# Kernel tuning notes

Measured on AMD Instinct MI355X. Metric: run time of the kernel, lower is better.

Reference implementation:

```python
import jax, jax.numpy as jnp
import numpy as np


def _apply_rope(t, cos, sin):
    # t: [b, s, h, d]; cos/sin: [s, d//2]; interleaved complex rotation
    b, s, h, d = t.shape
    tr = t.reshape(b, s, h, d // 2, 2)
    a, bb = tr[..., 0], tr[..., 1]
    c = cos[None, :, None, :]
    si = sin[None, :, None, :]
    out_r = a * c - bb * si
    out_i = a * si + bb * c
    return jnp.stack([out_r, out_i], axis=-1).reshape(b, s, h, d)


def setup_inputs() -> dict:
    key = jax.random.key(0)
    ks = jax.random.split(key, 10)
    B, S, D = 4, 512, 4096
    H, HKV, HD = 32, 8, 128
    START = 512
    wscale = 0.02  # keep activations in sane range
    x = jax.random.normal(ks[0], (B, S, D), dtype=jnp.float32)
    wq = jax.random.normal(ks[1], (H * HD, D), dtype=jnp.float32) * wscale
    wk = jax.random.normal(ks[2], (HKV * HD, D), dtype=jnp.float32) * wscale
    wv = jax.random.normal(ks[3], (HKV * HD, D), dtype=jnp.float32) * wscale
    wo = jax.random.normal(ks[4], (D, H * HD), dtype=jnp.float32) * wscale
    # RoPE angles for absolute positions [START, START+S)
    theta = 500000.0
    inv_freq = 1.0 / (theta ** (np.arange(0, HD, 2, dtype=np.float32) / HD))
    pos = np.arange(START, START + S, dtype=np.float32)
    ang = pos[:, None] * inv_freq[None, :]  # [S, HD//2]
    freqs_cos = jnp.asarray(np.cos(ang), dtype=jnp.float32)
    freqs_sin = jnp.asarray(np.sin(ang), dtype=jnp.float32)
    cache_k = jax.random.normal(ks[5], (B, START, HKV, HD), dtype=jnp.float32)
    cache_v = jax.random.normal(ks[6], (B, START, HKV, HD), dtype=jnp.float32)
    return {"x": x, "wq": wq, "wk": wk, "wv": wv, "wo": wo,
            "freqs_cos": freqs_cos, "freqs_sin": freqs_sin,
            "cache_k": cache_k, "cache_v": cache_v, "start_pos": START}


def reference(x, wq, wk, wv, wo, freqs_cos, freqs_sin, cache_k, cache_v, start_pos):
    B, S, D = x.shape
    H = wq.shape[0] // 128
    HKV = wk.shape[0] // 128
    HD = 128
    n_rep = H // HKV
    # QKV projections (Linear: y = x @ W^T)
    xq = jnp.einsum('bsd,ed->bse', x, wq).reshape(B, S, H, HD)
    xk = jnp.einsum('bsd,ed->bse', x, wk).reshape(B, S, HKV, HD)
    xv = jnp.einsum('bsd,ed->bse', x, wv).reshape(B, S, HKV, HD)
    # rotary embedding on new q/k
    xq = _apply_rope(xq, freqs_cos, freqs_sin)
    xk = _apply_rope(xk, freqs_cos, freqs_sin)
    # append new k/v to cache -> total kv length T = start_pos + S
    keys = jnp.concatenate([cache_k, xk], axis=1)    # [B, T, HKV, HD]
    values = jnp.concatenate([cache_v, xv], axis=1)  # [B, T, HKV, HD]
    # GQA: repeat kv heads (repeat_interleave along head dim)
    keys = jnp.repeat(keys, n_rep, axis=2)      # [B, T, H, HD]
    values = jnp.repeat(values, n_rep, axis=2)  # [B, T, H, HD]
    scores = jnp.einsum('bqhd,bkhd->bhqk', xq, keys) / jnp.sqrt(jnp.float32(HD))
    # causal mask: query abs pos start_pos+i attends to kv pos <= start_pos+i
    T = start_pos + S
    q_pos = start_pos + jnp.arange(S)
    k_pos = jnp.arange(T)
    mask = k_pos[None, :] <= q_pos[:, None]  # [S, T]
    scores = jnp.where(mask[None, None, :, :], scores, -jnp.inf)
    probs = jax.nn.softmax(scores.astype(jnp.float32), axis=-1).astype(x.dtype)
    out = jnp.einsum('bhqk,bkhd->bqhd', probs, values).reshape(B, S, H * HD)
    return jnp.einsum('bse,de->bsd', out, wo)
```

## Files before the change

### kernel.cpp

```cpp
#include <hip/hip_runtime.h>
#include <hip/hip_bf16.h>


#define B_ 4
#define S_ 512
#define D_ 4096
#define H_ 32
#define HKV_ 8
#define HD_ 128
#define T_ 1024
#define M_ 2048
#define NQKV_ 6144

typedef __attribute__((ext_vector_type(8))) short bf16x8;
typedef __attribute__((ext_vector_type(4))) float f32x4;

#define GLOAD_LDS16(g, l)                                                     \
  __builtin_amdgcn_global_load_lds(                                           \
      (const __attribute__((address_space(1))) void*)(g),                     \
      (__attribute__((address_space(3))) void*)(l), 16, 0, 0)

__global__ void cvt_f32_bf16(const float* __restrict__ in,
                             __hip_bfloat16* __restrict__ out, long n) {
  long i = ((long)blockIdx.x * blockDim.x + threadIdx.x) * 4;
  if (i >= n) return;
  float4 v = *(const float4*)(in + i);
  __hip_bfloat16 t[4] = {__float2bfloat16(v.x), __float2bfloat16(v.y),
                         __float2bfloat16(v.z), __float2bfloat16(v.w)};
  *(uint2*)(out + i) = *(const uint2*)t;
}

__global__ __launch_bounds__(512, 2) void gemm_qkv(
    const __hip_bfloat16* __restrict__ A, const __hip_bfloat16* __restrict__ B,
    float* __restrict__ C, int K, long ldA, long ldB, long ldC) {
  const int lin = blockIdx.x + 32 * blockIdx.y;
  const int swz = (lin & 7) * 32 + (lin >> 3);
  const int m0 = (swz >> 5) << 8;
  const int n0 = (swz & 31) * 192;

  const int tid = threadIdx.x;
  const int w = tid >> 6, l = tid & 63;
  const int wm = w >> 2, wn = w & 3;
  const int lr = l & 15, lq = l >> 4;

  __shared__ __align__(16) __hip_bfloat16 smem[2][28672];

  const int rS = w * 8 + (l >> 3);
  const int cS = (l & 7) ^ (l >> 3);
  const __hip_bfloat16* gA = A + (long)(m0 + rS) * ldA + cS * 8;
  const __hip_bfloat16* gB = B + (long)(n0 + rS) * ldB + cS * 8;
  const int wofs = w * 512;

  const int sl0 = (lq ^ (lr & 7)) * 8;
  const int sl1 = ((4 + lq) ^ (lr & 7)) * 8;
  const int aRow = (wm * 128 + lr) * 64;
  const int bRow = (wn * 48 + lr) * 64;

  f32x4 acc[8][3];
#pragma unroll
  for (int i = 0; i < 8; i++)
#pragma unroll
    for (int j = 0; j < 3; j++) acc[i][j] = f32x4{0.f, 0.f, 0.f, 0.f};

  const int nkt = K >> 6;

#define STAGEQ(buf, ko)                                              \
  {                                                                  \
    GLOAD_LDS16(gA + (ko), &smem[buf][wofs]);                        \
    GLOAD_LDS16(gA + 64 * ldA + (ko), &smem[buf][4096 + wofs]);      \
    GLOAD_LDS16(gA + 128 * ldA + (ko), &smem[buf][8192 + wofs]);     \
    GLOAD_LDS16(gA + 192 * ldA + (ko), &smem[buf][12288 + wofs]);    \
    GLOAD_LDS16(gB + (ko), &smem[buf][16384 + wofs]);                \
    GLOAD_LDS16(gB + 64 * ldB + (ko), &smem[buf][20480 + wofs]);     \
    GLOAD_LDS16(gB + 128 * ldB + (ko), &smem[buf][24576 + wofs]);    \
  }

  STAGEQ(0, 0);
  asm volatile("s_waitcnt vmcnt(0)" ::: "memory");
  __builtin_amdgcn_s_barrier();

  bf16x8 af[4], bfr[3];
  for (int t = 0; t < nkt; ++t) {
    const int bc = t & 1;
    int tn = t + 1;
    if (tn == nkt) tn = 0;
    const long ko = (long)tn << 6;
    const __hip_bfloat16* rA = &smem[bc][0];
    const __hip_bfloat16* rB = &smem[bc][16384];

#pragma unroll
    for (int i = 0; i < 4; i++)
      af[i] = *(const bf16x8*)(rA + aRow + i * 1024 + sl0);
#pragma unroll
    for (int j = 0; j < 3; j++)
      bfr[j] = *(const bf16x8*)(rB + bRow + j * 1024 + sl0);
    STAGEQ(bc ^ 1, ko);
    __builtin_amdgcn_s_barrier();
    __builtin_amdgcn_s_setprio(1);
#pragma unroll
    for (int i = 0; i < 4; i++)
#pragma unroll
      for (int j = 0; j < 3; j++)
        acc[i][j] = __builtin_amdgcn_mfma_f32_16x16x32_bf16(af[i], bfr[j],
                                                            acc[i][j], 0, 0, 0);
    __builtin_amdgcn_s_setprio(0);
    __builtin_amdgcn_s_barrier();

#pragma unroll
    for (int i = 0; i < 4; i++)
      af[i] = *(const bf16x8*)(rA + aRow + (i + 4) * 1024 + sl0);
    __builtin_amdgcn_s_barrier();
    __builtin_amdgcn_s_setprio(1);
#pragma unroll
    for (int i = 0; i < 4; i++)
#pragma unroll
      for (int j = 0; j < 3; j++)
        acc[i + 4][j] = __builtin_amdgcn_mfma_f32_16x16x32_bf16(
            af[i], bfr[j], acc[i + 4][j], 0, 0, 0);
    __builtin_amdgcn_s_setprio(0);
    __builtin_amdgcn_s_barrier();

#pragma unroll
    for (int i = 0; i < 4; i++)
      af[i] = *(const bf16x8*)(rA + aRow + i * 1024 + sl1);
#pragma unroll
    for (int j = 0; j < 3; j++)
      bfr[j] = *(const bf16x8*)(rB + bRow + j * 1024 + sl1);
    __builtin_amdgcn_s_barrier();
    __builtin_amdgcn_s_setprio(1);
#pragma unroll
    for (int i = 0; i < 4; i++)
#pragma unroll
      for (int j = 0; j < 3; j++)
        acc[i][j] = __builtin_amdgcn_mfma_f32_16x16x32_bf16(af[i], bfr[j],
                                                            acc[i][j], 0, 0, 0);
    __builtin_amdgcn_s_setprio(0);
    __builtin_amdgcn_s_barrier();

#pragma unroll
    for (int i = 0; i < 4; i++)
      af[i] = *(const bf16x8*)(rA + aRow + (i + 4) * 1024 + sl1);
    __builtin_amdgcn_s_barrier();
    __builtin_amdgcn_s_setprio(1);
#pragma unroll
    for (int i = 0; i < 4; i++)
#pragma unroll
      for (int j = 0; j < 3; j++)
        acc[i + 4][j] = __builtin_amdgcn_mfma_f32_16x16x32_bf16(
            af[i], bfr[j], acc[i + 4][j], 0, 0, 0);
    __builtin_amdgcn_s_setprio(0);
    asm volatile("s_waitcnt vmcnt(0)" ::: "memory");
    __builtin_amdgcn_s_barrier();
  }

#undef STAGEQ

  const int crow = m0 + wm * 128 + lq * 4;
  const int ccol = n0 + wn * 48 + lr;
#pragma unroll
  for (int i = 0; i < 8; i++)
#pragma unroll
    for (int j = 0; j < 3; j++)
#pragma unroll
      for (int r = 0; r < 4; r++)
        C[(long)(crow + i * 16 + r) * ldC + (ccol + j * 16)] = acc[i][j][r];
}

__global__ __launch_bounds__(512, 2) void gemm128(
    const __hip_bfloat16* __restrict__ A, const __hip_bfloat16* __restrict__ B,
    float* __restrict__ C, int M, int N, int K, long ldA, long ldB, long ldC) {
  const int nbx = N >> 8;
  const int nwg = nbx * (M >> 7);
  const int lin = blockIdx.x + nbx * blockIdx.y;
  const int cpx = nwg >> 3;
  const int swz = (lin & 7) * cpx + (lin >> 3);
  const int by = swz / nbx;
  const int m0 = by << 7;
  const int n0 = (swz - by * nbx) << 8;

  const int tid = threadIdx.x;
  const int w = tid >> 6, l = tid & 63;
  const int wm = w >> 2, wn = w & 3;
  const int lr = l & 15, lq = l >> 4;

  __shared__ __align__(16) __hip_bfloat16 smem[3][24576];

  const int rS = w * 16 + (l >> 2);
  const int cS = (l & 3) ^ ((rS >> 1) & 3);
  const __hip_bfloat16* gA = A + (long)(m0 + rS) * ldA + cS * 8;
  const __hip_bfloat16* gB = B + (long)(n0 + rS) * ldB + cS * 8;
  const long stB = 128 * ldB;
  const int wofs = w * 512;

  const int cR = (lq ^ ((lr >> 1) & 3)) * 8;
  const int aOff = (wm * 64 + lr) * 32 + cR;
  const int bOff = (wn * 64 + lr) * 32 + cR;

  f32x4 acc[4][4];
#pragma unroll
  for (int i = 0; i < 4; i++)
#pragma unroll
    for (int j = 0; j < 4; j++) acc[i][j] = f32x4{0.f, 0.f, 0.f, 0.f};

  const int nkt = K >> 6;

#define STAGEF(buf, ko)                                            \
  {                                                                \
    const __hip_bfloat16* ga_ = gA + (ko);                         \
    GLOAD_LDS16(ga_, &smem[buf][wofs]);                            \
    GLOAD_LDS16(ga_ + 32, &smem[buf][4096 + wofs]);                \
    const __hip_bfloat16* gb_ = gB + (ko);                         \
    GLOAD_LDS16(gb_, &smem[buf][8192 + wofs]);                     \
    GLOAD_LDS16(gb_ + stB, &smem[buf][12288 + wofs]);              \
    GLOAD_LDS16(gb_ + 32, &smem[buf][16384 + wofs]);               \
    GLOAD_LDS16(gb_ + stB + 32, &smem[buf][20480 + wofs]);         \
  }

  STAGEF(0, 0);
  STAGEF(1, 64);
  asm volatile("s_waitcnt vmcnt(6)" ::: "memory");
  __builtin_amdgcn_s_barrier();

  int bc = 0, b1 = 1, b2 = 2;
  bf16x8 af[4], bfr[4];
  for (int t = 0; t < nkt; ++t) {
    int t2 = t + 2;
    if (t2 >= nkt) t2 -= nkt;
    const long ko2 = (long)t2 << 6;
    STAGEF(b2, ko2);

    const __hip_bfloat16* rA = &smem[bc][0];
    const __hip_bfloat16* rB = &smem[bc][8192];

#pragma unroll
    for (int i = 0; i < 4; i++) af[i] = *(const bf16x8*)(rA + aOff + i * 512);
#pragma unroll
    for (int j = 0; j < 4; j++) bfr[j] = *(const bf16x8*)(rB + bOff + j * 512);
    __builtin_amdgcn_s_setprio(1);
#pragma unroll
    for (int i = 0; i < 4; i++)
#pragma unroll
      for (int j = 0; j < 4; j++)
        acc[i][j] = __builtin_amdgcn_mfma_f32_16x16x32_bf16(af[i], bfr[j],
                                                            acc[i][j], 0, 0, 0);
    __builtin_amdgcn_s_setprio(0);

#pragma unroll
    for (int i = 0; i < 4; i++)
      af[i] = *(const bf16x8*)(rA + 4096 + aOff + i * 512);
#pragma unroll
    for (int j = 0; j < 4; j++)
      bfr[j] = *(const bf16x8*)(rB + 8192 + bOff + j * 512);
    __builtin_amdgcn_s_setprio(1);
#pragma unroll
    for (int i = 0; i < 4; i++)
#pragma unroll
      for (int j = 0; j < 4; j++)
        acc[i][j] = __builtin_amdgcn_mfma_f32_16x16x32_bf16(af[i], bfr[j],
                                                            acc[i][j], 0, 0, 0);
    __builtin_amdgcn_s_setprio(0);

    asm volatile("s_waitcnt lgkmcnt(0)" ::: "memory");
    __builtin_amdgcn_sched_barrier(0);
    asm volatile("s_waitcnt vmcnt(6)" ::: "memory");
    __builtin_amdgcn_s_barrier();

    int tmp = bc; bc = b1; b1 = b2; b2 = tmp;
  }
  asm volatile("s_waitcnt vmcnt(0)" ::: "memory");

#undef STAGEF

  const int crow = m0 + wm * 64 + lq * 4;
  const int ccol = n0 + wn * 64 + lr;
#pragma unroll
  for (int i = 0; i < 4; i++)
#pragma unroll
    for (int j = 0; j < 4; j++)
#pragma unroll
      for (int r = 0; r < 4; r++)
        C[(long)(crow + i * 16 + r) * ldC + (ccol + j * 16)] = acc[i][j][r];
}

__global__ __launch_bounds__(256, 2) void flash_attn(
    const __hip_bfloat16* __restrict__ qb,
    const __hip_bfloat16* __restrict__ kb,
    const __hip_bfloat16* __restrict__ vtb,
    __hip_bfloat16* __restrict__ ob) {
  const int qt = 3 - blockIdx.x;
  const int z = blockIdx.y;
  const int b = z >> 5, h = z & 31, kvh = h >> 2;
  const int q0 = qt * 128;
  const int tid = threadIdx.x, wave = tid >> 6, lane = tid & 63;
  const int lr = lane & 15, lq = lane >> 4;
  const int wrow = wave * 32;
  const float scale = 0.08838834764831845f;

  __shared__ __align__(16) __hip_bfloat16 smem[64 * 128 + 128 * 64 + 128 * 72];
  __hip_bfloat16* Ks = smem;
  __hip_bfloat16* Vs = smem + 64 * 128;
  __hip_bfloat16* Ps = smem + 64 * 128 + 128 * 64;
  __hip_bfloat16* Os = smem;

  const __hip_bfloat16* Kz = kb + ((long)(b * 8 + kvh)) * T_ * HD_;
  const __hip_bfloat16* Vz = vtb + ((long)(b * 8 + kvh)) * HD_ * T_;
  const __hip_bfloat16* Qz = qb + ((long)(b * 512 + q0)) * 4096 + h * 128;
  __hip_bfloat16* obz = ob + ((long)(b * 512 + q0)) * 4096 + h * 128;

  bf16x8 qf[2][4];
#pragma unroll
  for (int i = 0; i < 2; i++)
#pragma unroll
    for (int kb4 = 0; kb4 < 4; kb4++)
      qf[i][kb4] = *(const bf16x8*)(Qz + (long)(wrow + i * 16 + lr) * 4096 +
                                    kb4 * 32 + lq * 8);

  int kOff[4], vOff[4];
#pragma unroll
  for (int it = 0; it < 4; it++) {
    int G = it * 256 + tid;
    int t = G >> 4, ck = (G & 15) ^ (t & 7);
    kOff[it] = t * 128 + ck * 8;
    int d = G >> 3, cv = (G & 7) ^ (d & 7);
    vOff[it] = d * 1024 + cv * 8;
  }

  f32x4 O[2][8];
#pragma unroll
  for (int i = 0; i < 2; i++)
#pragma unroll
    for (int j = 0; j < 8; j++) O[i][j] = f32x4{0.f, 0.f, 0.f, 0.f};
  float mst[2][4], lst[2][4];
#pragma unroll
  for (int i = 0; i < 2; i++)
#pragma unroll
    for (int r = 0; r < 4; r++) {
      mst[i][r] = -1e30f;
      lst[i][r] = 0.f;
    }

  const int ntiles = 10 + 2 * qt, fulltiles = 8 + 2 * qt;
  const int hxor = lr & 7;

  bf16x8 kreg[4], vreg[4];
#pragma unroll
  for (int it = 0; it < 4; it++)
    kreg[it] = *(const bf16x8*)(Kz + kOff[it]);
#pragma unroll
  for (int it = 0; it < 4; it++)
    vreg[it] = *(const bf16x8*)(Vz + vOff[it]);

  for (int kt = 0; kt < ntiles; kt++) {
    const int k0 = kt * 64;
#pragma unroll
    for (int it = 0; it < 4; it++)
      *(bf16x8*)(Ks + (it * 256 + tid) * 8) = kreg[it];
#pragma unroll
    for (int it = 0; it < 4; it++)
      *(bf16x8*)(Vs + (it * 256 + tid) * 8) = vreg[it];
    if (kt + 1 < ntiles) {
      const long kn = (long)(kt + 1) * 64;
#pragma unroll
      for (int it = 0; it < 4; it++)
        kreg[it] = *(const bf16x8*)(Kz + kn * 128 + kOff[it]);
#pragma unroll
      for (int it = 0; it < 4; it++)
        vreg[it] = *(const bf16x8*)(Vz + kn + vOff[it]);
    }
    asm volatile("s_waitcnt lgkmcnt(0)" ::: "memory");
    __builtin_amdgcn_s_barrier();

    f32x4 s[2][4];
#pragma unroll
    for (int i = 0; i < 2; i++)
#pragma unroll
      for (int j = 0; j < 4; j++) s[i][j] = f32x4{0.f, 0.f, 0.f, 0.f};
#pragma unroll
    for (int kb4 = 0; kb4 < 4; kb4++) {
      bf16x8 kf[4];
#pragma unroll
      for (int j = 0; j < 4; j++)
        kf[j] = *(const bf16x8*)(Ks + (j * 16 + lr) * 128 +
                                 ((kb4 * 4 + lq) ^ hxor) * 8);
#pragma unroll
      for (int i = 0; i < 2; i++)
#pragma unroll
        for (int j = 0; j < 4; j++)
          s[i][j] = __builtin_amdgcn_mfma_f32_16x16x32_bf16(qf[i][kb4], kf[j],
                                                            s[i][j], 0, 0, 0);
    }

    const bool mt = (kt >= fulltiles);
#pragma unroll
    for (int i = 0; i < 2; i++)
#pragma unroll
      for (int j = 0; j < 4; j++)
#pragma unroll
        for (int r = 0; r < 4; r++) {
          float sv = s[i][j][r] * scale;
          if (mt) {
            int key = k0 + j * 16 + lr;
            int qp = 512 + q0 + wrow + i * 16 + lq * 4 + r;
            if (key > qp) sv = -1e30f;
          }
          s[i][j][r] = sv;
        }

    float al[2][4];
#pragma unroll
    for (int i = 0; i < 2; i++)
#pragma unroll
      for (int r = 0; r < 4; r++) {
        float mx = fmaxf(fmaxf(s[i][0][r], s[i][1][r]),
                         fmaxf(s[i][2][r], s[i][3][r]));
        mx = fmaxf(mx, __shfl_xor(mx, 1));
        mx = fmaxf(mx, __shfl_xor(mx, 2));
        mx = fmaxf(mx, __shfl_xor(mx, 4));
        mx = fmaxf(mx, __shfl_xor(mx, 8));
        float mn = fmaxf(mst[i][r], mx);
        al[i][r] = __expf(mst[i][r] - mn);
        mst[i][r] = mn;
      }
#pragma unroll
    for (int i = 0; i < 2; i++)
#pragma unroll
      for (int j = 0; j < 4; j++)
#pragma unroll
        for (int r = 0; r < 4; r++)
          s[i][j][r] = __expf(s[i][j][r] - mst[i][r]);
#pragma unroll
    for (int i = 0; i < 2; i++)
#pragma unroll
      for (int r = 0; r < 4; r++) {
        float sm = s[i][0][r] + s[i][1][r] + s[i][2][r] + s[i][3][r];
        sm += __shfl_xor(sm, 1);
        sm += __shfl_xor(sm, 2);
        sm += __shfl_xor(sm, 4);
        sm += __shfl_xor(sm, 8);
        lst[i][r] = lst[i][r] * al[i][r] + sm;
      }
#pragma unroll
    for (int i = 0; i < 2; i++)
#pragma unroll
      for (int j = 0; j < 8; j++)
#pragma unroll
        for (int r = 0; r < 4; r++) O[i][j][r] *= al[i][r];

#pragma unroll
    for (int i = 0; i < 2; i++)
#pragma unroll
      for (int j = 0; j < 4; j++)
#pragma unroll
        for (int r = 0; r < 4; r++)
          Ps[(wrow + i * 16 + lq * 4 + r) * 72 + j * 16 + lr] =
              __float2bfloat16(s[i][j][r]);

#pragma unroll
    for (int kc = 0; kc < 2; kc++) {
      bf16x8 pa[2];
#pragma unroll
      for (int i = 0; i < 2; i++)
        pa[i] = *(const bf16x8*)(Ps + (wrow + i * 16 + lr) * 72 + kc * 32 +
                                 lq * 8);
      bf16x8 vf[8];
#pragma unroll
      for (int j = 0; j < 8; j++)
        vf[j] = *(const bf16x8*)(Vs + (j * 16 + lr) * 64 +
                                 ((kc * 4 + lq) ^ hxor) * 8);
#pragma unroll
      for (int i = 0; i < 2; i++)
#pragma unroll
        for (int j = 0; j < 8; j++)
          O[i][j] = __builtin_amdgcn_mfma_f32_16x16x32_bf16(pa[i], vf[j],
                                                            O[i][j], 0, 0, 0);
    }
    asm volatile("s_waitcnt lgkmcnt(0)" ::: "memory");
    __builtin_amdgcn_s_barrier();
  }

#pragma unroll
  for (int i = 0; i < 2; i++)
#pragma unroll
    for (int r = 0; r < 4; r++) {
      float inv = 1.f / lst[i][r];
#pragma unroll
      for (int j = 0; j < 8; j++)
        Os[(wrow + i * 16 + lq * 4 + r) * 136 + j * 16 + lr] =
            __float2bfloat16(O[i][j][r] * inv);
    }
  __syncthreads();
#pragma unroll
  for (int it = 0; it < 8; it++) {
    int G = it * 256 + tid;
    int m = G >> 4, c = G & 15;
    *(bf16x8*)(obz + (long)m * 4096 + c * 8) =
        *(const bf16x8*)(Os + m * 136 + c * 8);
  }
}

__global__ void rope_kernel(const float* __restrict__ qkv,
                            const float* __restrict__ fcos,
                            const float* __restrict__ fsin,
                            __hip_bfloat16* __restrict__ qb,
                            __hip_bfloat16* __restrict__ kb) {
  int m = blockIdx.y;
  int j = blockIdx.x * blockDim.x + threadIdx.x;
  if (j >= 2560) return;
  int s = m & (S_ - 1);
  long rowbase = (long)m * NQKV_;
  if (j < 2048) {
    int dpair = j & 63;
    float a = qkv[rowbase + 2 * j], bb = qkv[rowbase + 2 * j + 1];
    float c = fcos[s * 64 + dpair], si = fsin[s * 64 + dpair];
    long o = (long)m * 4096 + 2 * j;
    qb[o] = __float2bfloat16(a * c - bb * si);
    qb[o + 1] = __float2bfloat16(a * si + bb * c);
  } else {
    int j2 = j - 2048;
    int kvh = j2 >> 6, dpair = j2 & 63;
    float a = qkv[rowbase + 4096 + 2 * j2], bb = qkv[rowbase + 4096 + 2 * j2 + 1];
    float c = fcos[s * 64 + dpair], si = fsin[s * 64 + dpair];
    int b = m >> 9;
    long o = (((long)(b * HKV_ + kvh)) * T_ + 512 + s) * HD_ + 2 * dpair;
    kb[o] = __float2bfloat16(a * c - bb * si);
    kb[o + 1] = __float2bfloat16(a * si + bb * c);
  }
}

__global__ void kcache_cvt(const float* __restrict__ cache_k,
                           __hip_bfloat16* __restrict__ kb) {
  long i = (long)blockIdx.x * 256 + threadIdx.x;
  if (i >= (long)B_ * HKV_ * 512 * HD_) return;
  int d = i & 127;
  int t = (i >> 7) & 511;
  int kvh = (i >> 16) & 7;
  int b = i >> 19;
  long o = (((long)(b * HKV_ + kvh)) * T_ + t) * HD_ + d;
  kb[o] = __float2bfloat16(
      cache_k[(((long)(b * 512 + t)) * HKV_ + kvh) * HD_ + d]);
}

__global__ void v_transpose(const float* __restrict__ cache_v,
                            const float* __restrict__ qkv,
                            __hip_bfloat16* __restrict__ vtb) {
  __shared__ float tile[32][33];
  int t0 = blockIdx.x * 32, d0 = blockIdx.y * 32;
  int bk = blockIdx.z;
  int b = bk >> 3, kvh = bk & 7;
#pragma unroll
  for (int it = 0; it < 4; it++) {
    int t = t0 + threadIdx.y + it * 8;
    int d = d0 + threadIdx.x;
    float v;
    if (t < 512)
      v = cache_v[(((long)(b * 512 + t)) * HKV_ + kvh) * HD_ + d];
    else
      v = qkv[((long)(b * S_) + (t - 512)) * NQKV_ + 5120 + kvh * HD_ + d];
    tile[threadIdx.y + it * 8][threadIdx.x] = v;
  }
  __syncthreads();
#pragma unroll
  for (int it = 0; it < 4; it++) {
    int d = d0 + threadIdx.y + it * 8;
    int t = t0 + threadIdx.x;
    vtb[((long)bk * HD_ + d) * T_ + t] =
        __float2bfloat16(tile[threadIdx.x][threadIdx.y + it * 8]);
  }
}

extern "C" void kernel_launch(void* const* d_in, const int* in_sizes, int n_in,
                              void* d_out, int out_size, void* d_ws,
                              size_t ws_size, hipStream_t stream) {
  const float* x = (const float*)d_in[0];
  const float* wq = (const float*)d_in[1];
  const float* wk = (const float*)d_in[2];
  const float* wv = (const float*)d_in[3];
  const float* wo = (const float*)d_in[4];
  const float* fcos = (const float*)d_in[5];
  const float* fsin = (const float*)d_in[6];
  const float* cache_k = (const float*)d_in[7];
  const float* cache_v = (const float*)d_in[8];
  float* out = (float*)d_out;

  char* ws = (char*)d_ws;
  const size_t szR0 = (size_t)M_ * 4096 * 2;
  const size_t szR1 = (size_t)NQKV_ * D_ * 2;
  const size_t szR2 = (size_t)M_ * NQKV_ * 4;
  const size_t szKV = (size_t)B_ * HKV_ * T_ * HD_ * 2;

  size_t R0 = 0;
  size_t R1 = R0 + szR0;
  size_t R2 = R1 + szR1;
  size_t R3 = R2 + szR2;
  size_t R4 = R3 + szKV;

  __hip_bfloat16* xb = (__hip_bfloat16*)(ws + R0);
  __hip_bfloat16* wqkvb = (__hip_bfloat16*)(ws + R1);
  float* qkvf = (float*)(ws + R2);
  __hip_bfloat16* kb = (__hip_bfloat16*)(ws + R3);
  __hip_bfloat16* vtb = (__hip_bfloat16*)(ws + R4);

  dim3 blk(256);

  cvt_f32_bf16<<<(M_ * (long)D_ / 4 + 255) / 256, blk, 0, stream>>>(
      x, xb, (long)M_ * D_);
  cvt_f32_bf16<<<((long)D_ * D_ / 4 + 255) / 256, blk, 0, stream>>>(
      wq, wqkvb, (long)D_ * D_);
  cvt_f32_bf16<<<((long)1024 * D_ / 4 + 255) / 256, blk, 0, stream>>>(
      wk, wqkvb + (long)4096 * D_, (long)1024 * D_);
  cvt_f32_bf16<<<((long)1024 * D_ / 4 + 255) / 256, blk, 0, stream>>>(
      wv, wqkvb + (long)5120 * D_, (long)1024 * D_);

  gemm_qkv<<<dim3(32, 8), dim3(512), 0, stream>>>(
      xb, wqkvb, qkvf, D_, D_, D_, NQKV_);

  __hip_bfloat16* qb = xb;
  rope_kernel<<<dim3(10, M_), blk, 0, stream>>>(qkvf, fcos, fsin, qb, kb);

  kcache_cvt<<<((long)B_ * HKV_ * 512 * HD_ + 255) / 256, blk, 0, stream>>>(
      cache_k, kb);
  v_transpose<<<dim3(T_ / 32, HD_ / 32, B_ * HKV_), dim3(32, 8), 0, stream>>>(
      cache_v, qkvf, vtb);

  __hip_bfloat16* wob = wqkvb;
  cvt_f32_bf16<<<((long)D_ * D_ / 4 + 255) / 256, blk, 0, stream>>>(
      wo, wob, (long)D_ * D_);

  __hip_bfloat16* ob = xb;
  flash_attn<<<dim3(4, B_ * H_), blk, 0, stream>>>(qb, kb, vtb, ob);

  gemm128<<<dim3(D_ / 256, M_ / 128), dim3(512), 0, stream>>>(
      ob, wob, out, M_, D_, D_, D_, D_, D_);
}
```

Measured before the change: 500.0 us.

## Shrink attention query tile to 64, load K/V direct-to-LDS, lazy softmax rescale, fuse weight converts

Flash attention now uses 64-query tiles (one 16-row MFMA block per wave) with twice as many blocks and a 4-blocks-per-CU launch bound. The P buffer reuses the K region to cut shared memory. K/V tiles load with global_load_lds instead of register prefetch, which drops the software pipelining and adds an extra barrier per tile. Softmax skips the running-max rescale while the new max stays within 8 of the old one. The three Q/K/V weight conversions become a single kernel launch.

```diff
diff --git a/kernel.cpp b/kernel.cpp
--- a/kernel.cpp
+++ b/kernel.cpp
@@ -25,6 +25,27 @@
   long i = ((long)blockIdx.x * blockDim.x + threadIdx.x) * 4;
   if (i >= n) return;
   float4 v = *(const float4*)(in + i);
+  __hip_bfloat16 t[4] = {__float2bfloat16(v.x), __float2bfloat16(v.y),
+                         __float2bfloat16(v.z), __float2bfloat16(v.w)};
+  *(uint2*)(out + i) = *(const uint2*)t;
+}
+
+__global__ void cvt_wqkv(const float* __restrict__ wq,
+                         const float* __restrict__ wk,
+                         const float* __restrict__ wv,
+                         __hip_bfloat16* __restrict__ out) {
+  long i = ((long)blockIdx.x * 256 + threadIdx.x) * 4;
+  long row = i >> 12;
+  const float* src;
+  long off;
+  if (row < 4096) {
+    src = wq; off = i;
+  } else if (row < 5120) {
+    src = wk; off = i - (long)4096 * 4096;
+  } else {
+    src = wv; off = i - (long)5120 * 4096;
+  }
+  float4 v = *(const float4*)(src + off);
   __hip_bfloat16 t[4] = {__float2bfloat16(v.x), __float2bfloat16(v.y),
                          __float2bfloat16(v.z), __float2bfloat16(v.w)};
   *(uint2*)(out + i) = *(const uint2*)t;
@@ -282,24 +303,24 @@
         C[(long)(crow + i * 16 + r) * ldC + (ccol + j * 16)] = acc[i][j][r];
 }
 
-__global__ __launch_bounds__(256, 2) void flash_attn(
+__global__ __launch_bounds__(256, 4) void flash_attn(
     const __hip_bfloat16* __restrict__ qb,
     const __hip_bfloat16* __restrict__ kb,
     const __hip_bfloat16* __restrict__ vtb,
     __hip_bfloat16* __restrict__ ob) {
-  const int qt = 3 - blockIdx.x;
+  const int qt = 7 - blockIdx.x;
   const int z = blockIdx.y;
   const int b = z >> 5, h = z & 31, kvh = h >> 2;
-  const int q0 = qt * 128;
+  const int q0 = qt * 64;
   const int tid = threadIdx.x, wave = tid >> 6, lane = tid & 63;
   const int lr = lane & 15, lq = lane >> 4;
-  const int wrow = wave * 32;
+  const int wrow = wave * 16;
   const float scale = 0.08838834764831845f;
 
-  __shared__ __align__(16) __hip_bfloat16 smem[64 * 128 + 128 * 64 + 128 * 72];
+  __shared__ __align__(16) __hip_bfloat16 smem[64 * 128 + 128 * 64];
   __hip_bfloat16* Ks = smem;
   __hip_bfloat16* Vs = smem + 64 * 128;
-  __hip_bfloat16* Ps = smem + 64 * 128 + 128 * 64;
+  __hip_bfloat16* Ps = smem;
   __hip_bfloat16* Os = smem;
 
   const __hip_bfloat16* Kz = kb + ((long)(b * 8 + kvh)) * T_ * HD_;
@@ -307,13 +328,11 @@
   const __hip_bfloat16* Qz = qb + ((long)(b * 512 + q0)) * 4096 + h * 128;
   __hip_bfloat16* obz = ob + ((long)(b * 512 + q0)) * 4096 + h * 128;
 
-  bf16x8 qf[2][4];
-#pragma unroll
-  for (int i = 0; i < 2; i++)
-#pragma unroll
-    for (int kb4 = 0; kb4 < 4; kb4++)
-      qf[i][kb4] = *(const bf16x8*)(Qz + (long)(wrow + i * 16 + lr) * 4096 +
-                                    kb4 * 32 + lq * 8);
+  bf16x8 qf[4];
+#pragma unroll
+  for (int kb4 = 0; kb4 < 4; kb4++)
+    qf[kb4] = *(const bf16x8*)(Qz + (long)(wrow + lr) * 4096 + kb4 * 32 +
+                               lq * 8);
 
   int kOff[4], vOff[4];
 #pragma unroll
@@ -325,56 +344,33 @@
     vOff[it] = d * 1024 + cv * 8;
   }
 
-  f32x4 O[2][8];
-#pragma unroll
-  for (int i = 0; i < 2; i++)
-#pragma unroll
-    for (int j = 0; j < 8; j++) O[i][j] = f32x4{0.f, 0.f, 0.f, 0.f};
-  float mst[2][4], lst[2][4];
-#pragma unroll
-  for (int i = 0; i < 2; i++)
-#pragma unroll
-    for (int r = 0; r < 4; r++) {
-      mst[i][r] = -1e30f;
-      lst[i][r] = 0.f;
-    }
-
-  const int ntiles = 10 + 2 * qt, fulltiles = 8 + 2 * qt;
+  f32x4 O[8];
+#pragma unroll
+  for (int j = 0; j < 8; j++) O[j] = f32x4{0.f, 0.f, 0.f, 0.f};
+  float mst[4], lst[4];
+#pragma unroll
+  for (int r = 0; r < 4; r++) {
+    mst[r] = -1e30f;
+    lst[r] = 0.f;
+  }
+
+  const int ntiles = 9 + qt, fulltiles = 8 + qt;
   const int hxor = lr & 7;
-
-  bf16x8 kreg[4], vreg[4];
-#pragma unroll
-  for (int it = 0; it < 4; it++)
-    kreg[it] = *(const bf16x8*)(Kz + kOff[it]);
-#pragma unroll
-  for (int it = 0; it < 4; it++)
-    vreg[it] = *(const bf16x8*)(Vz + vOff[it]);
 
   for (int kt = 0; kt < ntiles; kt++) {
     const int k0 = kt * 64;
 #pragma unroll
     for (int it = 0; it < 4; it++)
-      *(bf16x8*)(Ks + (it * 256 + tid) * 8) = kreg[it];
+      GLOAD_LDS16(Kz + (long)k0 * 128 + kOff[it],
+                  Ks + (it * 256 + wave * 64) * 8);
 #pragma unroll
     for (int it = 0; it < 4; it++)
-      *(bf16x8*)(Vs + (it * 256 + tid) * 8) = vreg[it];
-    if (kt + 1 < ntiles) {
-      const long kn = (long)(kt + 1) * 64;
-#pragma unroll
-      for (int it = 0; it < 4; it++)
-        kreg[it] = *(const bf16x8*)(Kz + kn * 128 + kOff[it]);
-#pragma unroll
-      for (int it = 0; it < 4; it++)
-        vreg[it] = *(const bf16x8*)(Vz + kn + vOff[it]);
-    }
-    asm volatile("s_waitcnt lgkmcnt(0)" ::: "memory");
-    __builtin_amdgcn_s_barrier();
-
-    f32x4 s[2][4];
-#pragma unroll
-    for (int i = 0; i < 2; i++)
-#pragma unroll
-      for (int j = 0; j < 4; j++) s[i][j] = f32x4{0.f, 0.f, 0.f, 0.f};
+      GLOAD_LDS16(Vz + k0 + vOff[it], Vs + (it * 256 + wave * 64) * 8);
+    __syncthreads();
+
+    f32x4 s[4];
+#pragma unroll
+    for (int j = 0; j < 4; j++) s[j] = f32x4{0.f, 0.f, 0.f, 0.f};
 #pragma unroll
     for (int kb4 = 0; kb4 < 4; kb4++) {
       bf16x8 kf[4];
@@ -383,114 +379,113 @@
         kf[j] = *(const bf16x8*)(Ks + (j * 16 + lr) * 128 +
                                  ((kb4 * 4 + lq) ^ hxor) * 8);
 #pragma unroll
-      for (int i = 0; i < 2; i++)
-#pragma unroll
-        for (int j = 0; j < 4; j++)
-          s[i][j] = __builtin_amdgcn_mfma_f32_16x16x32_bf16(qf[i][kb4], kf[j],
-                                                            s[i][j], 0, 0, 0);
+      for (int j = 0; j < 4; j++)
+        s[j] = __builtin_amdgcn_mfma_f32_16x16x32_bf16(qf[kb4], kf[j], s[j],
+                                                       0, 0, 0);
     }
+    __syncthreads();
 
     const bool mt = (kt >= fulltiles);
 #pragma unroll
-    for (int i = 0; i < 2; i++)
+    for (int j = 0; j < 4; j++)
+#pragma unroll
+      for (int r = 0; r < 4; r++) {
+        float sv = s[j][r] * scale;
+        if (mt) {
+          int key = k0 + j * 16 + lr;
+          int qp = 512 + q0 + wrow + lq * 4 + r;
+          if (key > qp) sv = -1e30f;
+        }
+        s[j][r] = sv;
+      }
+
+    float mx[4];
+    bool ok = true;
+#pragma unroll
+    for (int r = 0; r < 4; r++) {
+      float m = fmaxf(fmaxf(s[0][r], s[1][r]), fmaxf(s[2][r], s[3][r]));
+      m = fmaxf(m, __shfl_xor(m, 1));
+      m = fmaxf(m, __shfl_xor(m, 2));
+      m = fmaxf(m, __shfl_xor(m, 4));
+      m = fmaxf(m, __shfl_xor(m, 8));
+      mx[r] = m;
+      ok = ok && (m - mst[r] <= 8.f);
+    }
+    if (__all(ok)) {
 #pragma unroll
       for (int j = 0; j < 4; j++)
 #pragma unroll
-        for (int r = 0; r < 4; r++) {
-          float sv = s[i][j][r] * scale;
-          if (mt) {
-            int key = k0 + j * 16 + lr;
-            int qp = 512 + q0 + wrow + i * 16 + lq * 4 + r;
-            if (key > qp) sv = -1e30f;
-          }
-          s[i][j][r] = sv;
-        }
-
-    float al[2][4];
-#pragma unroll
-    for (int i = 0; i < 2; i++)
+        for (int r = 0; r < 4; r++) s[j][r] = __expf(s[j][r] - mst[r]);
 #pragma unroll
       for (int r = 0; r < 4; r++) {
-        float mx = fmaxf(fmaxf(s[i][0][r], s[i][1][r]),
-                         fmaxf(s[i][2][r], s[i][3][r]));
-        mx = fmaxf(mx, __shfl_xor(mx, 1));
-        mx = fmaxf(mx, __shfl_xor(mx, 2));
-        mx = fmaxf(mx, __shfl_xor(mx, 4));
-        mx = fmaxf(mx, __shfl_xor(mx, 8));
-        float mn = fmaxf(mst[i][r], mx);
-        al[i][r] = __expf(mst[i][r] - mn);
-        mst[i][r] = mn;
-      }
-#pragma unroll
-    for (int i = 0; i < 2; i++)
-#pragma unroll
-      for (int j = 0; j < 4; j++)
-#pragma unroll
-        for (int r = 0; r < 4; r++)
-          s[i][j][r] = __expf(s[i][j][r] - mst[i][r]);
-#pragma unroll
-    for (int i = 0; i < 2; i++)
-#pragma unroll
-      for (int r = 0; r < 4; r++) {
-        float sm = s[i][0][r] + s[i][1][r] + s[i][2][r] + s[i][3][r];
+        float sm = s[0][r] + s[1][r] + s[2][r] + s[3][r];
         sm += __shfl_xor(sm, 1);
         sm += __shfl_xor(sm, 2);
         sm += __shfl_xor(sm, 4);
         sm += __shfl_xor(sm, 8);
-        lst[i][r] = lst[i][r] * al[i][r] + sm;
+        lst[r] += sm;
       }
-#pragma unroll
-    for (int i = 0; i < 2; i++)
+    } else {
+      float al[4];
+#pragma unroll
+      for (int r = 0; r < 4; r++) {
+        float mn = fmaxf(mst[r], mx[r]);
+        al[r] = __expf(mst[r] - mn);
+        mst[r] = mn;
+      }
+#pragma unroll
+      for (int j = 0; j < 4; j++)
+#pragma unroll
+        for (int r = 0; r < 4; r++) s[j][r] = __expf(s[j][r] - mst[r]);
+#pragma unroll
+      for (int r = 0; r < 4; r++) {
+        float sm = s[0][r] + s[1][r] + s[2][r] + s[3][r];
+        sm += __shfl_xor(sm, 1);
+        sm += __shfl_xor(sm, 2);
+        sm += __shfl_xor(sm, 4);
+        sm += __shfl_xor(sm, 8);
+        lst[r] = lst[r] * al[r] + sm;
+      }
 #pragma unroll
       for (int j = 0; j < 8; j++)
 #pragma unroll
-        for (int r = 0; r < 4; r++) O[i][j][r] *= al[i][r];
-
-#pragma unroll
-    for (int i = 0; i < 2; i++)
-#pragma unroll
-      for (int j = 0; j < 4; j++)
-#pragma unroll
-        for (int r = 0; r < 4; r++)
-          Ps[(wrow + i * 16 + lq * 4 + r) * 72 + j * 16 + lr] =
-              __float2bfloat16(s[i][j][r]);
+        for (int r = 0; r < 4; r++) O[j][r] *= al[r];
+    }
+
+#pragma unroll
+    for (int j = 0; j < 4; j++)
+#pragma unroll
+      for (int r = 0; r < 4; r++)
+        Ps[(wrow + lq * 4 + r) * 72 + j * 16 + lr] = __float2bfloat16(s[j][r]);
 
 #pragma unroll
     for (int kc = 0; kc < 2; kc++) {
-      bf16x8 pa[2];
-#pragma unroll
-      for (int i = 0; i < 2; i++)
-        pa[i] = *(const bf16x8*)(Ps + (wrow + i * 16 + lr) * 72 + kc * 32 +
-                                 lq * 8);
+      bf16x8 pa =
+          *(const bf16x8*)(Ps + (wrow + lr) * 72 + kc * 32 + lq * 8);
       bf16x8 vf[8];
 #pragma unroll
       for (int j = 0; j < 8; j++)
         vf[j] = *(const bf16x8*)(Vs + (j * 16 + lr) * 64 +
                                  ((kc * 4 + lq) ^ hxor) * 8);
 #pragma unroll
-      for (int i = 0; i < 2; i++)
-#pragma unroll
-        for (int j = 0; j < 8; j++)
-          O[i][j] = __builtin_amdgcn_mfma_f32_16x16x32_bf16(pa[i], vf[j],
-                                                            O[i][j], 0, 0, 0);
+      for (int j = 0; j < 8; j++)
+        O[j] = __builtin_amdgcn_mfma_f32_16x16x32_bf16(pa, vf[j], O[j],
+                                                       0, 0, 0);
     }
-    asm volatile("s_waitcnt lgkmcnt(0)" ::: "memory");
-    __builtin_amdgcn_s_barrier();
-  }
-
-#pragma unroll
-  for (int i = 0; i < 2; i++)
-#pragma unroll
-    for (int r = 0; r < 4; r++) {
-      float inv = 1.f / lst[i][r];
-#pragma unroll
-      for (int j = 0; j < 8; j++)
-        Os[(wrow + i * 16 + lq * 4 + r) * 136 + j * 16 + lr] =
-            __float2bfloat16(O[i][j][r] * inv);
-    }
+    __syncthreads();
+  }
+
+#pragma unroll
+  for (int r = 0; r < 4; r++) {
+    float inv = 1.f / lst[r];
+#pragma unroll
+    for (int j = 0; j < 8; j++)
+      Os[(wrow + lq * 4 + r) * 136 + j * 16 + lr] =
+          __float2bfloat16(O[j][r] * inv);
+  }
   __syncthreads();
 #pragma unroll
-  for (int it = 0; it < 8; it++) {
+  for (int it = 0; it < 4; it++) {
     int G = it * 256 + tid;
     int m = G >> 4, c = G & 15;
     *(bf16x8*)(obz + (long)m * 4096 + c * 8) =
@@ -604,12 +599,8 @@
 
   cvt_f32_bf16<<<(M_ * (long)D_ / 4 + 255) / 256, blk, 0, stream>>>(
       x, xb, (long)M_ * D_);
-  cvt_f32_bf16<<<((long)D_ * D_ / 4 + 255) / 256, blk, 0, stream>>>(
-      wq, wqkvb, (long)D_ * D_);
-  cvt_f32_bf16<<<((long)1024 * D_ / 4 + 255) / 256, blk, 0, stream>>>(
-      wk, wqkvb + (long)4096 * D_, (long)1024 * D_);
-  cvt_f32_bf16<<<((long)1024 * D_ / 4 + 255) / 256, blk, 0, stream>>>(
-      wv, wqkvb + (long)5120 * D_, (long)1024 * D_);
+  cvt_wqkv<<<((long)NQKV_ * D_ / 4 + 255) / 256, blk, 0, stream>>>(
+      wq, wk, wv, wqkvb);
 
   gemm_qkv<<<dim3(32, 8), dim3(512), 0, stream>>>(
       xb, wqkvb, qkvf, D_, D_, D_, NQKV_);
@@ -627,7 +618,7 @@
       wo, wob, (long)D_ * D_);
 
   __hip_bfloat16* ob = xb;
-  flash_attn<<<dim3(4, B_ * H_), blk, 0, stream>>>(qb, kb, vtb, ob);
+  flash_attn<<<dim3(8, B_ * H_), blk, 0, stream>>>(qb, kb, vtb, ob);
 
   gemm128<<<dim3(D_ / 256, M_ / 128), dim3(512), 0, stream>>>(
       ob, wob, out, M_, D_, D_, D_, D_, D_);
```

Result: slower. 565.7 us (+13.1%).
